# Performance work log

Hardware: AMD Instinct MI355X
Metric: run time of the kernel (lower is better)

## Reference

```python
import jax, jax.numpy as jnp
import numpy as np

B, S, D, H, FF = 2, 2048, 1024, 16, 4096
HD = D // H
EPS = 1e-5


def _ln(x, g, b):
    m = jnp.mean(x, axis=-1, keepdims=True)
    v = jnp.mean((x - m) ** 2, axis=-1, keepdims=True)
    return (x - m) * jax.lax.rsqrt(v + EPS) * g + b


def _rope(x, cos, sin):
    # non-standard RoPE: split full d_model at half, rotate (pre head-split)
    half = x.shape[-1] // 2
    x1, x2 = x[..., :half], x[..., half:]
    return jnp.concatenate([x1 * cos - x2 * sin, x1 * sin + x2 * cos], axis=-1)


def _heads(x, b, s):
    return x.reshape(b, s, H, HD).transpose(0, 2, 1, 3)  # [b,h,s,hd]


def _attn(q, k, v):
    scores = jnp.einsum('bhqd,bhkd->bhqk', q, k) / jnp.sqrt(jnp.float32(HD))
    w = jax.nn.softmax(scores, axis=-1)
    return jnp.einsum('bhqk,bhkd->bhqd', w, v)


def setup_inputs() -> dict:
    key = jax.random.key(0)
    ks = jax.random.split(key, 32)
    sc = 0.02
    d = {
        'x': jax.random.normal(ks[0], (B, S, D), jnp.float32),
        'cond_emb': jax.random.normal(ks[1], (B, D), jnp.float32),
    }
    # proper RoPE tables over half_dim = D//2
    pos = np.arange(S)[:, None]
    inv = 1.0 / (10000.0 ** (np.arange(D // 2) / (D // 2)))
    ang = pos * inv[None, :]
    d['cos_pos'] = jnp.asarray(np.cos(ang), jnp.float32)
    d['sin_pos'] = jnp.asarray(np.sin(ang), jnp.float32)
    names = ['Wq', 'Wk', 'Wv', 'Wo', 'Wqc', 'Wkc', 'Wvc', 'Woc']
    for i, n in enumerate(names):
        d[n] = jax.random.normal(ks[2 + i], (D, D), jnp.float32) * sc
        d['b' + n[1:]] = jnp.zeros((D,), jnp.float32)
    d['W1'] = jax.random.normal(ks[12], (D, FF), jnp.float32) * sc
    d['b1'] = jnp.zeros((FF,), jnp.float32)
    d['W2'] = jax.random.normal(ks[13], (FF, D), jnp.float32) * sc
    d['b2'] = jnp.zeros((D,), jnp.float32)
    for i in (1, 2, 3):
        d[f'g{i}'] = jnp.ones((D,), jnp.float32)
        d[f'be{i}'] = jnp.zeros((D,), jnp.float32)
    return d


def reference(x, cond_emb, cos_pos, sin_pos,
              Wq, bq, Wk, bk, Wv, bv, Wo, bo,
              Wqc, bqc, Wkc, bkc, Wvc, bvc, Woc, boc,
              W1, b1, W2, b2, g1, be1, g2, be2, g3, be3):
    b, s, _ = x.shape
    # self-attention with RoPE applied on full d_model before head split
    residual = x
    xn = _ln(x, g1, be1)
    q = _rope(xn @ Wq + bq, cos_pos, sin_pos)
    k = _rope(xn @ Wk + bk, cos_pos, sin_pos)
    v = xn @ Wv + bv
    o = _attn(_heads(q, b, s), _heads(k, b, s), _heads(v, b, s))
    o = o.transpose(0, 2, 1, 3).reshape(b, s, D) @ Wo + bo
    x = residual + o
    # cross-attention with single-token context
    residual = x
    xn = _ln(x, g2, be2)
    cond = cond_emb[:, None, :]  # [b,1,D]
    qc = _heads(xn @ Wqc + bqc, b, s)
    kc = _heads(cond @ Wkc + bkc, b, 1)
    vc = _heads(cond @ Wvc + bvc, b, 1)
    oc = _attn(qc, kc, vc)
    oc = oc.transpose(0, 2, 1, 3).reshape(b, s, D) @ Woc + boc
    x = residual + oc
    # FFN (exact GELU)
    residual = x
    xn = _ln(x, g3, be3)
    h = jax.nn.gelu(xn @ W1 + b1, approximate=False)
    return residual + (h @ W2 + b2)
```

## Files before the change

kernel.cpp:

```cpp
#include <hip/hip_runtime.h>
#include <cmath>

#define B_  2
#define S_  2048
#define D_  1024
#define H_  16
#define HD_ 64
#define FF_ 4096
#define M_  4096

typedef __attribute__((ext_vector_type(8))) __bf16 bf16x8;
typedef __attribute__((ext_vector_type(4))) __bf16 bf16x4;
typedef __attribute__((ext_vector_type(4))) float  f32x4;

__device__ __forceinline__ void gload_lds16(void* lds, const void* g) {
    __builtin_amdgcn_global_load_lds(
        (const __attribute__((address_space(1))) unsigned int*)g,
        (__attribute__((address_space(3))) unsigned int*)lds,
        16, 0, 0);
}

#define FENCE() asm volatile("" ::: "memory")

__global__ __launch_bounds__(256)
void tcast(const float* __restrict__ src, __bf16* __restrict__ dst, int K, int N)
{
    __shared__ float t[32][33];
    int tx = threadIdx.x & 31, ty = threadIdx.x >> 5;
    int k0 = blockIdx.y * 32, n0 = blockIdx.x * 32;
#pragma unroll
    for (int i = 0; i < 4; ++i)
        t[ty + i * 8][tx] = src[(size_t)(k0 + ty + i * 8) * N + n0 + tx];
    __syncthreads();
#pragma unroll
    for (int i = 0; i < 4; ++i)
        dst[(size_t)(n0 + ty + i * 8) * K + k0 + tx] = (__bf16)t[tx][ty + i * 8];
}

__global__ __launch_bounds__(256)
void tcast3(const float* __restrict__ wa, const float* __restrict__ wb,
            const float* __restrict__ wc, __bf16* __restrict__ dstb)
{
    __shared__ float t[32][33];
    const float* src = blockIdx.z == 0 ? wa : (blockIdx.z == 1 ? wb : wc);
    __bf16* dst = dstb + (size_t)blockIdx.z * 1024 * 1024;
    int tx = threadIdx.x & 31, ty = threadIdx.x >> 5;
    int k0 = blockIdx.y * 32, n0 = blockIdx.x * 32;
#pragma unroll
    for (int i = 0; i < 4; ++i)
        t[ty + i * 8][tx] = src[(size_t)(k0 + ty + i * 8) * 1024 + n0 + tx];
    __syncthreads();
#pragma unroll
    for (int i = 0; i < 4; ++i)
        dst[(size_t)(n0 + ty + i * 8) * 1024 + k0 + tx] = (__bf16)t[tx][ty + i * 8];
}

__global__ __launch_bounds__(256)
void catb(const float* __restrict__ a, const float* __restrict__ b,
          const float* __restrict__ c, float* __restrict__ o)
{
    int i = blockIdx.x * 256 + threadIdx.x;
    o[i] = i < 1024 ? a[i] : (i < 2048 ? b[i - 1024] : c[i - 2048]);
}

__global__ __launch_bounds__(256)
void colgemv(const float* __restrict__ inp, const float* __restrict__ W,
             const float* __restrict__ bias, float* __restrict__ out, int K, int N)
{
    __shared__ float part[4][16];
    const int b = blockIdx.y;
    const int t = threadIdx.x;
    const int w = t >> 6, lane = t & 63;
    const int colIdx = lane & 15;
    const int col = blockIdx.x * 16 + colIdx;
    const int ks = w * 4 + (lane >> 4);
    const int kpt = K >> 4;
    const float* ip = inp + (size_t)b * K + ks * kpt;
    const float* wp = W + (size_t)ks * kpt * N + col;
    float acc = 0.f;
#pragma unroll 8
    for (int i = 0; i < kpt; ++i)
        acc += ip[i] * wp[(size_t)i * N];
    acc += __shfl_xor(acc, 16);
    acc += __shfl_xor(acc, 32);
    if (lane < 16) part[w][colIdx] = acc;
    __syncthreads();
    if (t < 16) {
        float r = part[0][t] + part[1][t] + part[2][t] + part[3][t]
                + bias[blockIdx.x * 16 + t];
        out[(size_t)b * N + blockIdx.x * 16 + t] = r;
    }
}

__global__ __launch_bounds__(256)
void ln_cast(const float* __restrict__ x, const float* __restrict__ g,
             const float* __restrict__ be, __bf16* __restrict__ out)
{
    int row = blockIdx.x, tid = threadIdx.x;
    const float4* xp = (const float4*)(x + (size_t)row * D_);
    float4 v = xp[tid];
    float s  = v.x + v.y + v.z + v.w;
    float s2 = v.x * v.x + v.y * v.y + v.z * v.z + v.w * v.w;
#pragma unroll
    for (int off = 32; off > 0; off >>= 1) {
        s  += __shfl_down(s, off);
        s2 += __shfl_down(s2, off);
    }
    __shared__ float rs[4], rs2[4];
    int wid = tid >> 6, lane = tid & 63;
    if (lane == 0) { rs[wid] = s; rs2[wid] = s2; }
    __syncthreads();
    float tot  = rs[0] + rs[1] + rs[2] + rs[3];
    float tot2 = rs2[0] + rs2[1] + rs2[2] + rs2[3];
    float mean = tot * (1.0f / D_);
    float var  = tot2 * (1.0f / D_) - mean * mean;
    float rstd = rsqrtf(var + 1e-5f);
    float4 gv = ((const float4*)g)[tid];
    float4 bv = ((const float4*)be)[tid];
    bf16x4 ov;
    ov[0] = (__bf16)((v.x - mean) * rstd * gv.x + bv.x);
    ov[1] = (__bf16)((v.y - mean) * rstd * gv.y + bv.y);
    ov[2] = (__bf16)((v.z - mean) * rstd * gv.z + bv.z);
    ov[3] = (__bf16)((v.w - mean) * rstd * gv.w + bv.w);
    ((bf16x4*)(out + (size_t)row * D_))[tid] = ov;
}

__global__ __launch_bounds__(128)
void rope_qk(const __bf16* __restrict__ qkv, const float* __restrict__ cosp,
             const float* __restrict__ sinp, __bf16* __restrict__ Qh,
             __bf16* __restrict__ Kh)
{
    int row = blockIdx.x, tid = threadIdx.x;
    int b = row >> 11, s = row & 2047;
    float4 c  = ((const float4*)(cosp + (size_t)s * 512))[tid];
    float4 sn = ((const float4*)(sinp + (size_t)s * 512))[tid];
    int d0 = tid * 4;
    int h1 = d0 >> 6, dd = d0 & 63;
#pragma unroll
    for (int which = 0; which < 2; ++which) {
        const int off = which * 1024;
        const float scale = which ? 1.0f : 0.125f;
        __bf16* out = which ? Kh : Qh;
        bf16x4 a  = *(const bf16x4*)(qkv + (size_t)row * 3072 + off + tid * 4);
        bf16x4 bb = *(const bf16x4*)(qkv + (size_t)row * 3072 + off + 512 + tid * 4);
        float x1a = (float)a[0],  x1b = (float)a[1],  x1c = (float)a[2],  x1d = (float)a[3];
        float x2a = (float)bb[0], x2b = (float)bb[1], x2c = (float)bb[2], x2d = (float)bb[3];
        bf16x4 o1, o2;
        o1[0] = (__bf16)((x1a * c.x - x2a * sn.x) * scale);
        o1[1] = (__bf16)((x1b * c.y - x2b * sn.y) * scale);
        o1[2] = (__bf16)((x1c * c.z - x2c * sn.z) * scale);
        o1[3] = (__bf16)((x1d * c.w - x2d * sn.w) * scale);
        o2[0] = (__bf16)((x1a * sn.x + x2a * c.x) * scale);
        o2[1] = (__bf16)((x1b * sn.y + x2b * c.y) * scale);
        o2[2] = (__bf16)((x1c * sn.z + x2c * c.z) * scale);
        o2[3] = (__bf16)((x1d * sn.w + x2d * c.w) * scale);
        *(bf16x4*)(out + ((size_t)((b * H_ + h1) * S_ + s) * HD_) + dd) = o1;
        *(bf16x4*)(out + ((size_t)((b * H_ + h1 + 8) * S_ + s) * HD_) + dd) = o2;
    }
}

__global__ __launch_bounds__(256)
void vtrans2(const __bf16* __restrict__ qkv, __bf16* __restrict__ Vt)
{
    __shared__ __bf16 t[32][33];
    int tx = threadIdx.x & 31, ty = threadIdx.x >> 5;
    int bh = blockIdx.z;
    int b = bh >> 4, h = bh & 15;
    int s0 = blockIdx.y * 32, d0 = blockIdx.x * 32;
    __bf16* dst = Vt + (size_t)bh * HD_ * S_;
#pragma unroll
    for (int i = 0; i < 4; ++i)
        t[ty + i * 8][tx] = qkv[(size_t)(b * 2048 + s0 + ty + i * 8) * 3072
                                + 2048 + h * 64 + d0 + tx];
    __syncthreads();
#pragma unroll
    for (int i = 0; i < 4; ++i)
        dst[(size_t)(d0 + ty + i * 8) * S_ + s0 + tx] = t[tx][ty + i * 8];
}

template<int EPI>
__global__ __launch_bounds__(512)
void gemm8(const __bf16* __restrict__ A, const __bf16* __restrict__ Bt,
           const float* __restrict__ bias, __bf16* __restrict__ o0,
           __bf16* __restrict__ o1, int M, int N, int K, int klen)
{
    __shared__ __align__(16) char smem[131072];
    const int tid = threadIdx.x;
    const int wid = tid >> 6, lane = tid & 63;
    const int l15 = lane & 15, l16 = lane >> 4;
    const int wm = wid >> 2, wn = wid & 3;

    const int gx = gridDim.x;
    const int nwg = gx * gridDim.y;
    int wg = blockIdx.y * gx + blockIdx.x;
    wg = (wg & 7) * (nwg >> 3) + (wg >> 3);
    const int n0 = (wg % gx) * 256;
    const int m0 = (wg / gx) * 256;
    const int kz = blockIdx.z * klen;
    const size_t K2 = (size_t)K * 2;

    const int srow = tid >> 3;
    const int scol = ((tid & 7) * 16) ^ ((srow & 7) << 4);
    const char* gA = (const char*)A + (size_t)(m0 + srow) * K2 + (size_t)kz * 2 + scol;
    const char* gB = (const char*)Bt + (size_t)(n0 + srow) * K2 + (size_t)kz * 2 + scol;

    auto stageA = [&](int c) {
        char* d = (char*)smem + c * 32768 + wid * 1024;
        gload_lds16(d,         gA);
        gload_lds16(d + 8192,  gA + 64 * K2);
        gload_lds16(d + 16384, gA + 128 * K2);
        gload_lds16(d + 24576, gA + 192 * K2);
    };
    auto stageB = [&](int c) {
        char* d = (char*)smem + 65536 + c * 32768 + wid * 1024;
        gload_lds16(d,         gB);
        gload_lds16(d + 8192,  gB + 64 * K2);
        gload_lds16(d + 16384, gB + 128 * K2);
        gload_lds16(d + 24576, gB + 192 * K2);
    };

    const int sw = (l15 & 7) << 4;
    const int x0 = (l16 * 16) ^ sw;
    const int x1 = (64 + l16 * 16) ^ sw;
    const int aoff = (wm * 128 + l15) * 128;
    const int boff = 65536 + (wn * 64 + l15) * 128;

    f32x4 acc[8][4] = {};
    const int NT = klen >> 6;

    stageA(0); stageB(0); gA += 128; gB += 128;
    stageA(1); stageB(1); gA += 128; gB += 128;
    asm volatile("s_waitcnt vmcnt(8)" ::: "memory");
    __builtin_amdgcn_s_barrier();

    for (int t = 0; t < NT; ++t) {
        const int cur = t & 1;
        const char* sa = (const char*)smem + cur * 32768;
        const bool pf = (t + 2) < NT;

        bf16x8 af0[8], af1[8];
        bf16x8 b00, b01, b02, b03, b10, b11, b12, b13;

#pragma unroll
        for (int mi = 0; mi < 8; ++mi)
            af0[mi] = *(const bf16x8*)(sa + aoff + mi * 2048 + x0);
        b00 = *(const bf16x8*)(sa + boff + 0 * 2048 + x0);
        b01 = *(const bf16x8*)(sa + boff + 1 * 2048 + x0);
        FENCE();
        __builtin_amdgcn_s_barrier();
        __builtin_amdgcn_s_setprio(1);
#pragma unroll
        for (int mi = 0; mi < 8; ++mi) {
            acc[mi][0] = __builtin_amdgcn_mfma_f32_16x16x32_bf16(af0[mi], b00, acc[mi][0], 0, 0, 0);
            acc[mi][1] = __builtin_amdgcn_mfma_f32_16x16x32_bf16(af0[mi], b01, acc[mi][1], 0, 0, 0);
        }
        __builtin_amdgcn_s_setprio(0);

#pragma unroll
        for (int mi = 0; mi < 8; ++mi)
            af1[mi] = *(const bf16x8*)(sa + aoff + mi * 2048 + x1);
        b02 = *(const bf16x8*)(sa + boff + 2 * 2048 + x0);
        b03 = *(const bf16x8*)(sa + boff + 3 * 2048 + x0);
        FENCE();
        __builtin_amdgcn_s_barrier();
        __builtin_amdgcn_s_setprio(1);
#pragma unroll
        for (int mi = 0; mi < 8; ++mi) {
            acc[mi][2] = __builtin_amdgcn_mfma_f32_16x16x32_bf16(af0[mi], b02, acc[mi][2], 0, 0, 0);
            acc[mi][3] = __builtin_amdgcn_mfma_f32_16x16x32_bf16(af0[mi], b03, acc[mi][3], 0, 0, 0);
        }
        __builtin_amdgcn_s_setprio(0);

        b10 = *(const bf16x8*)(sa + boff + 0 * 2048 + x1);
        b11 = *(const bf16x8*)(sa + boff + 1 * 2048 + x1);
        FENCE();
        __builtin_amdgcn_s_barrier();
        if (pf) stageA(cur);
        __builtin_amdgcn_s_setprio(1);
#pragma unroll
        for (int mi = 0; mi < 8; ++mi) {
            acc[mi][0] = __builtin_amdgcn_mfma_f32_16x16x32_bf16(af1[mi], b10, acc[mi][0], 0, 0, 0);
            acc[mi][1] = __builtin_amdgcn_mfma_f32_16x16x32_bf16(af1[mi], b11, acc[mi][1], 0, 0, 0);
        }
        __builtin_amdgcn_s_setprio(0);

        b12 = *(const bf16x8*)(sa + boff + 2 * 2048 + x1);
        b13 = *(const bf16x8*)(sa + boff + 3 * 2048 + x1);
        FENCE();
        __builtin_amdgcn_s_barrier();
        if (pf) { stageB(cur); gA += 128; gB += 128; }
        __builtin_amdgcn_s_setprio(1);
#pragma unroll
        for (int mi = 0; mi < 8; ++mi) {
            acc[mi][2] = __builtin_amdgcn_mfma_f32_16x16x32_bf16(af1[mi], b12, acc[mi][2], 0, 0, 0);
            acc[mi][3] = __builtin_amdgcn_mfma_f32_16x16x32_bf16(af1[mi], b13, acc[mi][3], 0, 0, 0);
        }
        __builtin_amdgcn_s_setprio(0);
        if (pf) asm volatile("s_waitcnt vmcnt(8)" ::: "memory");
        else    asm volatile("s_waitcnt vmcnt(0)" ::: "memory");
        __builtin_amdgcn_s_barrier();
        FENCE();
    }

#pragma unroll
    for (int mi = 0; mi < 8; ++mi)
#pragma unroll
        for (int ni = 0; ni < 4; ++ni) {
            int gc = n0 + wn * 64 + ni * 16 + l15;
            float bb = (EPI == 2) ? 0.f : bias[gc];
#pragma unroll
            for (int r = 0; r < 4; ++r) {
                int gr = m0 + wm * 128 + mi * 16 + l16 * 4 + r;
                float v = acc[mi][ni][r] + bb;
                if constexpr (EPI == 0) {
                    o0[(size_t)gr * N + gc] = (__bf16)v;
                } else if constexpr (EPI == 1) {
                    o0[(size_t)gr * N + gc] =
                        (__bf16)(0.5f * v * (1.0f + erff(v * 0.70710678118f)));
                } else {
                    const size_t PSZ = (size_t)M_ * 1024;
                    __bf16* po = (blockIdx.z < 2) ? (o0 + blockIdx.z * PSZ)
                                                  : (o1 + (blockIdx.z - 2) * PSZ);
                    po[(size_t)gr * N + gc] = (__bf16)v;
                }
            }
        }
}

__global__ __launch_bounds__(256)
void ffn2_red(const __bf16* __restrict__ pA, const __bf16* __restrict__ pB,
              const float* __restrict__ x2, const float* __restrict__ b2,
              float* __restrict__ out)
{
    const size_t PSZ = (size_t)M_ * 1024;
    size_t i = ((size_t)blockIdx.x * 256 + threadIdx.x) * 8;
    bf16x8 a0 = *(const bf16x8*)(pA + i);
    bf16x8 a1 = *(const bf16x8*)(pA + PSZ + i);
    bf16x8 c0 = *(const bf16x8*)(pB + i);
    bf16x8 c1 = *(const bf16x8*)(pB + PSZ + i);
    float4 xa = *(const float4*)(x2 + i);
    float4 xb = *(const float4*)(x2 + i + 4);
    float xs[8] = {xa.x, xa.y, xa.z, xa.w, xb.x, xb.y, xb.z, xb.w};
#pragma unroll
    for (int j = 0; j < 8; ++j) {
        int col = (int)((i + j) & 1023);
        out[i + j] = xs[j] + b2[col]
                   + (float)a0[j] + (float)a1[j] + (float)c0[j] + (float)c1[j];
    }
}

__global__ __launch_bounds__(256)
void gemm_bt(const __bf16* __restrict__ A, const __bf16* __restrict__ Bt,
             const float* __restrict__ bias, const float* __restrict__ resid,
             const float* __restrict__ extra, float* __restrict__ outF,
             int M, int N, int K)
{
    __shared__ __align__(16) __bf16 As[128 * 64];
    __shared__ __align__(16) __bf16 Bs[128 * 64];
    const int tid = threadIdx.x;
    const int wid = tid >> 6, lane = tid & 63;
    const int m0 = blockIdx.y * 128, n0 = blockIdx.x * 128;
    const int wm = wid >> 1, wn = wid & 1;
    const int l15 = lane & 15, l16 = lane >> 4;

    f32x4 acc[4][4] = {};
    char* asb = (char*)As;
    char* bsb = (char*)Bs;
    const char* ag = (const char*)A;
    const char* bg = (const char*)Bt;
    const int srow = lane >> 3;
    const int scolsw = ((lane & 7) * 16) ^ (srow << 4);

    for (int k0 = 0; k0 < K; k0 += 64) {
        __syncthreads();
#pragma unroll
        for (int i = 0; i < 4; ++i) {
            int j = wid * 4 + i;
            int row = j * 8 + srow;
            gload_lds16(asb + j * 1024,
                        ag + (size_t)(m0 + row) * (K * 2) + k0 * 2 + scolsw);
        }
#pragma unroll
        for (int i = 0; i < 4; ++i) {
            int j = wid * 4 + i;
            int row = j * 8 + srow;
            gload_lds16(bsb + j * 1024,
                        bg + (size_t)(n0 + row) * (K * 2) + k0 * 2 + scolsw);
        }
        __syncthreads();

        bf16x8 af[4][2], bfr[4][2];
#pragma unroll
        for (int mi = 0; mi < 4; ++mi) {
            int row = wm * 64 + mi * 16 + l15;
            int swl = (row & 7) << 4;
#pragma unroll
            for (int kk = 0; kk < 2; ++kk)
                af[mi][kk] = *(const bf16x8*)(asb + row * 128 + ((l16 * 16 + kk * 64) ^ swl));
        }
#pragma unroll
        for (int ni = 0; ni < 4; ++ni) {
            int row = wn * 64 + ni * 16 + l15;
            int swl = (row & 7) << 4;
#pragma unroll
            for (int kk = 0; kk < 2; ++kk)
                bfr[ni][kk] = *(const bf16x8*)(bsb + row * 128 + ((l16 * 16 + kk * 64) ^ swl));
        }
#pragma unroll
        for (int mi = 0; mi < 4; ++mi)
#pragma unroll
            for (int ni = 0; ni < 4; ++ni) {
                acc[mi][ni] = __builtin_amdgcn_mfma_f32_16x16x32_bf16(af[mi][0], bfr[ni][0], acc[mi][ni], 0, 0, 0);
                acc[mi][ni] = __builtin_amdgcn_mfma_f32_16x16x32_bf16(af[mi][1], bfr[ni][1], acc[mi][ni], 0, 0, 0);
            }
    }

#pragma unroll
    for (int mi = 0; mi < 4; ++mi)
#pragma unroll
        for (int ni = 0; ni < 4; ++ni) {
            int gc = n0 + wn * 64 + ni * 16 + l15;
            float bb = bias[gc];
#pragma unroll
            for (int r = 0; r < 4; ++r) {
                int gr = m0 + wm * 64 + mi * 16 + l16 * 4 + r;
                float v = acc[mi][ni][r] + bb;
                size_t idx = (size_t)gr * N + gc;
                int b = gr >> 11;
                outF[idx] = resid[idx] + v + extra[(size_t)b * N + gc];
            }
        }
}

__global__ __launch_bounds__(256)
void attn_fwd(const __bf16* __restrict__ Qh, const __bf16* __restrict__ Kh,
              const __bf16* __restrict__ Vt, __bf16* __restrict__ O)
{
    __shared__ __align__(16) char smem[40960];
    const int tid = threadIdx.x, wid = tid >> 6, lane = tid & 63;
    const int l15 = lane & 15, l16 = lane >> 4;

    const int wg = blockIdx.x;
    const int rr = wg >> 3;
    const int qb = rr & 31;
    const int bh = (wg & 7) + 8 * (rr >> 5);

    const int q0 = qb * 64 + wid * 16;
    const size_t qkbase = (size_t)bh * S_ * HD_;

    bf16x8 qf[2];
    {
        const __bf16* qp = Qh + qkbase + (size_t)(q0 + l15) * HD_ + l16 * 8;
        qf[0] = *(const bf16x8*)qp;
        qf[1] = *(const bf16x8*)(qp + 32);
    }
    float m = -1e30f, sum = 0.f;
    f32x4 o[4] = {};
    const int srow = lane >> 3;
    const int scolsw = ((lane & 7) * 16) ^ (srow << 4);
    const char* kg = (const char*)(Kh + qkbase);
    const char* vg = (const char*)(Vt + (size_t)bh * HD_ * S_);

    auto stage = [&](int c, int t) {
        int s0 = t * 64;
#pragma unroll
        for (int cc = 0; cc < 2; ++cc) {
            int j = wid * 2 + cc;
            int row = j * 8 + srow;
            gload_lds16(smem + c * 8192 + j * 1024,
                        kg + (size_t)(s0 + row) * 128 + scolsw);
            gload_lds16(smem + 16384 + c * 8192 + j * 1024,
                        vg + (size_t)row * (S_ * 2) + s0 * 2 + scolsw);
        }
    };

    const int NT = S_ / 64;
    stage(0, 0);
    stage(1, 1);
    asm volatile("s_waitcnt vmcnt(4)" ::: "memory");
    __builtin_amdgcn_s_barrier();

    for (int kt = 0; kt < NT; ++kt) {
        const int cur = kt & 1;
        const char* Kl = smem + cur * 8192;
        const char* Vl = smem + 16384 + cur * 8192;
        char* Pl = smem + 32768;

        f32x4 st[4];
        __builtin_amdgcn_s_setprio(1);
#pragma unroll
        for (int t = 0; t < 4; ++t) {
            int row = t * 16 + l15;
            int swl = (row & 7) << 4;
            bf16x8 ak0 = *(const bf16x8*)(Kl + row * 128 + ((l16 * 16) ^ swl));
            bf16x8 ak1 = *(const bf16x8*)(Kl + row * 128 + ((l16 * 16 + 64) ^ swl));
            f32x4 z = {0.f, 0.f, 0.f, 0.f};
            z = __builtin_amdgcn_mfma_f32_16x16x32_bf16(ak0, qf[0], z, 0, 0, 0);
            st[t] = __builtin_amdgcn_mfma_f32_16x16x32_bf16(ak1, qf[1], z, 0, 0, 0);
        }
        __builtin_amdgcn_s_setprio(0);

        float rmax = -1e30f;
#pragma unroll
        for (int t = 0; t < 4; ++t)
#pragma unroll
            for (int r = 0; r < 4; ++r) rmax = fmaxf(rmax, st[t][r]);
        rmax = fmaxf(rmax, __shfl_xor(rmax, 16));
        rmax = fmaxf(rmax, __shfl_xor(rmax, 32));
        if (!__all(rmax <= m + 8.f)) {
            float mnew = fmaxf(m, rmax);
            float corr = __expf(m - mnew);
            sum *= corr;
            float c0 = __shfl(corr, l16 * 4 + 0);
            float c1 = __shfl(corr, l16 * 4 + 1);
            float c2 = __shfl(corr, l16 * 4 + 2);
            float c3 = __shfl(corr, l16 * 4 + 3);
#pragma unroll
            for (int dg = 0; dg < 4; ++dg) {
                o[dg][0] *= c0; o[dg][1] *= c1; o[dg][2] *= c2; o[dg][3] *= c3;
            }
            m = mnew;
        }
        float rsum = 0.f;
        float p[4][4];
#pragma unroll
        for (int t = 0; t < 4; ++t)
#pragma unroll
            for (int r = 0; r < 4; ++r) { p[t][r] = __expf(st[t][r] - m); rsum += p[t][r]; }
        rsum += __shfl_xor(rsum, 16);
        rsum += __shfl_xor(rsum, 32);
        sum += rsum;

        {
            char* pw = Pl + wid * 2048 + l15 * 128;
            int swl = (l15 & 7) << 4;
#pragma unroll
            for (int t = 0; t < 4; ++t) {
                bf16x4 pk;
                pk[0] = (__bf16)p[t][0]; pk[1] = (__bf16)p[t][1];
                pk[2] = (__bf16)p[t][2]; pk[3] = (__bf16)p[t][3];
                *(bf16x4*)(pw + ((t * 32 + l16 * 8) ^ swl)) = pk;
            }
        }
        {
            const char* pr = Pl + wid * 2048 + l15 * 128;
            int swp = (l15 & 7) << 4;
            bf16x8 ap0 = *(const bf16x8*)(pr + ((l16 * 16) ^ swp));
            bf16x8 ap1 = *(const bf16x8*)(pr + ((l16 * 16 + 64) ^ swp));
            __builtin_amdgcn_s_setprio(1);
#pragma unroll
            for (int dg = 0; dg < 4; ++dg) {
                int row = dg * 16 + l15;
                int swl = (row & 7) << 4;
                bf16x8 bv0 = *(const bf16x8*)(Vl + row * 128 + ((l16 * 16) ^ swl));
                bf16x8 bv1 = *(const bf16x8*)(Vl + row * 128 + ((l16 * 16 + 64) ^ swl));
                o[dg] = __builtin_amdgcn_mfma_f32_16x16x32_bf16(ap0, bv0, o[dg], 0, 0, 0);
                o[dg] = __builtin_amdgcn_mfma_f32_16x16x32_bf16(ap1, bv1, o[dg], 0, 0, 0);
            }
            __builtin_amdgcn_s_setprio(0);
        }

        FENCE();
        __builtin_amdgcn_s_barrier();
        if (kt + 2 < NT) {
            stage(cur, kt + 2);
            asm volatile("s_waitcnt vmcnt(4)" ::: "memory");
        } else {
            asm volatile("s_waitcnt vmcnt(0)" ::: "memory");
        }
        __builtin_amdgcn_s_barrier();
        FENCE();
    }

    int b = bh >> 4, hh = bh & 15;
#pragma unroll
    for (int r = 0; r < 4; ++r) {
        float inv = 1.0f / __shfl(sum, l16 * 4 + r);
        int qg = q0 + l16 * 4 + r;
        __bf16* op = O + ((size_t)(b * S_ + qg) * D_) + hh * HD_;
#pragma unroll
        for (int dg = 0; dg < 4; ++dg)
            op[dg * 16 + l15] = (__bf16)(o[dg][r] * inv);
    }
}

extern "C" void kernel_launch(void* const* d_in, const int* in_sizes, int n_in,
                              void* d_out, int out_size, void* d_ws, size_t ws_size,
                              hipStream_t stream)
{
    (void)in_sizes; (void)n_in; (void)out_size; (void)ws_size;
    const float* x    = (const float*)d_in[0];
    const float* cond = (const float*)d_in[1];
    const float* cosp = (const float*)d_in[2];
    const float* sinp = (const float*)d_in[3];
    const float* Wq = (const float*)d_in[4];  const float* bq = (const float*)d_in[5];
    const float* Wk = (const float*)d_in[6];  const float* bk = (const float*)d_in[7];
    const float* Wv = (const float*)d_in[8];  const float* bv = (const float*)d_in[9];
    const float* Wo = (const float*)d_in[10]; const float* bo = (const float*)d_in[11];
    const float* Wvc = (const float*)d_in[16]; const float* bvc = (const float*)d_in[17];
    const float* Woc = (const float*)d_in[18]; const float* boc = (const float*)d_in[19];
    const float* W1 = (const float*)d_in[20]; const float* b1 = (const float*)d_in[21];
    const float* W2 = (const float*)d_in[22]; const float* b2 = (const float*)d_in[23];
    const float* g1 = (const float*)d_in[24]; const float* be1 = (const float*)d_in[25];
    const float* g3 = (const float*)d_in[28]; const float* be3 = (const float*)d_in[29];

    char* ws = (char*)d_ws;
    const size_t MB = 1ull << 20;
    __bf16* WqkvT = (__bf16*)(ws + 0 * MB);
    __bf16* WoT   = (__bf16*)(ws + 6 * MB);
    __bf16* W1T   = (__bf16*)(ws + 8 * MB);
    __bf16* W2T   = (__bf16*)(ws + 16 * MB);
    __bf16* xn    = (__bf16*)(ws + 24 * MB);
    __bf16* qkvh  = (__bf16*)(ws + 32 * MB);
    __bf16* Qh    = (__bf16*)(ws + 56 * MB);
    __bf16* Kh    = (__bf16*)(ws + 64 * MB);
    __bf16* Vt    = (__bf16*)(ws + 72 * MB);
    __bf16* oflat = (__bf16*)(ws + 80 * MB);
    float*  bqkv  = (float*)(ws + 88 * MB);
    float*  vc    = (float*)(ws + 88 * MB + 16384);
    float*  ocp   = (float*)(ws + 88 * MB + 32768);
    float*  x2    = (float*)(ws + 32 * MB);
    __bf16* hbuf  = (__bf16*)(ws + 48 * MB);
    __bf16* pA    = (__bf16*)(ws + 0 * MB);
    __bf16* pB    = (__bf16*)(ws + 80 * MB);

    tcast3<<<dim3(32, 32, 3), 256, 0, stream>>>(Wq, Wk, Wv, WqkvT);
    tcast<<<dim3(32, 32),  256, 0, stream>>>(Wo, WoT, 1024, 1024);
    tcast<<<dim3(128, 32), 256, 0, stream>>>(W1, W1T, 1024, 4096);
    tcast<<<dim3(32, 128), 256, 0, stream>>>(W2, W2T, 4096, 1024);
    catb<<<12, 256, 0, stream>>>(bq, bk, bv, bqkv);
    colgemv<<<dim3(64, 2), 256, 0, stream>>>(cond, Wvc, bvc, vc, 1024, 1024);
    colgemv<<<dim3(64, 2), 256, 0, stream>>>(vc, Woc, boc, ocp, 1024, 1024);
    ln_cast<<<M_, 256, 0, stream>>>(x, g1, be1, xn);
    gemm8<0><<<dim3(12, 16, 1), 512, 0, stream>>>(xn, WqkvT, bqkv, qkvh, nullptr,
                                                  M_, 3072, 1024, 1024);
    rope_qk<<<M_, 128, 0, stream>>>(qkvh, cosp, sinp, Qh, Kh);
    vtrans2<<<dim3(2, 64, 32), 256, 0, stream>>>(qkvh, Vt);
    attn_fwd<<<1024, 256, 0, stream>>>(Qh, Kh, Vt, oflat);
    gemm_bt<<<dim3(8, 32), 256, 0, stream>>>(oflat, WoT, bo, x, ocp, x2,
                                             M_, 1024, 1024);
    ln_cast<<<M_, 256, 0, stream>>>(x2, g3, be3, xn);
    gemm8<1><<<dim3(16, 16, 1), 512, 0, stream>>>(xn, W1T, b1, hbuf, nullptr,
                                                  M_, 4096, 1024, 1024);
    gemm8<2><<<dim3(4, 16, 4), 512, 0, stream>>>(hbuf, W2T, nullptr, pA, pB,
                                                 M_, 1024, 4096, 1024);
    ffn2_red<<<2048, 256, 0, stream>>>(pA, pB, x2, b2, (float*)d_out);
}
```

Before: 274.3 us.

## Rewrite attention with 32x32 MFMA tiles, register-resident P, exp2 softmax

The flash-attention kernel moves from 16x16x32 to 32x32x16 MFMA tiles, so each wave handles 32 queries and each block 128, halving the grid. The P matrix no longer round-trips through shared memory: it is packed to bf16 in registers and rearranged with cross-half lane shuffles to form the B operand of the PV MFMA. Softmax switches to exp2 by folding log2(e) into the Q scale inside the RoPE kernel, and the lazy-rescale threshold is widened to match. This removes LDS traffic and per-row shuffles for the rescale factors, at the cost of more registers per wave and fewer blocks, which may lower occupancy.

```diff
diff --git a/kernel.cpp b/kernel.cpp
--- a/kernel.cpp
+++ b/kernel.cpp
@@ -12,6 +12,8 @@
 typedef __attribute__((ext_vector_type(8))) __bf16 bf16x8;
 typedef __attribute__((ext_vector_type(4))) __bf16 bf16x4;
 typedef __attribute__((ext_vector_type(4))) float  f32x4;
+typedef __attribute__((ext_vector_type(16))) float f32x16;
+typedef __attribute__((ext_vector_type(4))) unsigned u32x4;
 
 __device__ __forceinline__ void gload_lds16(void* lds, const void* g) {
     __builtin_amdgcn_global_load_lds(
@@ -21,6 +23,12 @@
 }
 
 #define FENCE() asm volatile("" ::: "memory")
+
+__device__ __forceinline__ unsigned pk_bf16(float lo, float hi) {
+    unsigned short lu = __builtin_bit_cast(unsigned short, (__bf16)lo);
+    unsigned short hu = __builtin_bit_cast(unsigned short, (__bf16)hi);
+    return (unsigned)lu | ((unsigned)hu << 16);
+}
 
 __global__ __launch_bounds__(256)
 void tcast(const float* __restrict__ src, __bf16* __restrict__ dst, int K, int N)
@@ -139,7 +147,7 @@
 #pragma unroll
     for (int which = 0; which < 2; ++which) {
         const int off = which * 1024;
-        const float scale = which ? 1.0f : 0.125f;
+        const float scale = which ? 1.0f : 0.18033688f;
         __bf16* out = which ? Kh : Qh;
         bf16x4 a  = *(const bf16x4*)(qkv + (size_t)row * 3072 + off + tid * 4);
         bf16x4 bb = *(const bf16x4*)(qkv + (size_t)row * 3072 + off + 512 + tid * 4);
@@ -436,28 +444,31 @@
 void attn_fwd(const __bf16* __restrict__ Qh, const __bf16* __restrict__ Kh,
               const __bf16* __restrict__ Vt, __bf16* __restrict__ O)
 {
-    __shared__ __align__(16) char smem[40960];
+    __shared__ __align__(16) char smem[32768];
     const int tid = threadIdx.x, wid = tid >> 6, lane = tid & 63;
-    const int l15 = lane & 15, l16 = lane >> 4;
+    const int l31 = lane & 31, hi = lane >> 5;
 
     const int wg = blockIdx.x;
     const int rr = wg >> 3;
-    const int qb = rr & 31;
-    const int bh = (wg & 7) + 8 * (rr >> 5);
-
-    const int q0 = qb * 64 + wid * 16;
+    const int qb = rr & 15;
+    const int bh = (wg & 7) + 8 * (rr >> 4);
+
+    const int qg = qb * 128 + wid * 32 + l31;
     const size_t qkbase = (size_t)bh * S_ * HD_;
 
-    bf16x8 qf[2];
+    bf16x8 qf[4];
     {
-        const __bf16* qp = Qh + qkbase + (size_t)(q0 + l15) * HD_ + l16 * 8;
-        qf[0] = *(const bf16x8*)qp;
-        qf[1] = *(const bf16x8*)(qp + 32);
-    }
+        const __bf16* qp = Qh + qkbase + (size_t)qg * HD_ + hi * 8;
+#pragma unroll
+        for (int kh = 0; kh < 4; ++kh)
+            qf[kh] = *(const bf16x8*)(qp + kh * 16);
+    }
+
     float m = -1e30f, sum = 0.f;
-    f32x4 o[4] = {};
+    f32x16 acc0 = {}, acc1 = {};
+
     const int srow = lane >> 3;
-    const int scolsw = ((lane & 7) * 16) ^ (srow << 4);
+    const int scolsw = ((lane & 7) * 16) ^ ((srow & 7) << 4);
     const char* kg = (const char*)(Kh + qkbase);
     const char* vg = (const char*)(Vt + (size_t)bh * HD_ * S_);
 
@@ -474,6 +485,8 @@
         }
     };
 
+    const int swz0 = (l31 & 7) << 4;
+
     const int NT = S_ / 64;
     stage(0, 0);
     stage(1, 1);
@@ -484,81 +497,72 @@
         const int cur = kt & 1;
         const char* Kl = smem + cur * 8192;
         const char* Vl = smem + 16384 + cur * 8192;
-        char* Pl = smem + 32768;
-
-        f32x4 st[4];
+
+        f32x16 st0 = {}, st1 = {};
         __builtin_amdgcn_s_setprio(1);
 #pragma unroll
-        for (int t = 0; t < 4; ++t) {
-            int row = t * 16 + l15;
-            int swl = (row & 7) << 4;
-            bf16x8 ak0 = *(const bf16x8*)(Kl + row * 128 + ((l16 * 16) ^ swl));
-            bf16x8 ak1 = *(const bf16x8*)(Kl + row * 128 + ((l16 * 16 + 64) ^ swl));
-            f32x4 z = {0.f, 0.f, 0.f, 0.f};
-            z = __builtin_amdgcn_mfma_f32_16x16x32_bf16(ak0, qf[0], z, 0, 0, 0);
-            st[t] = __builtin_amdgcn_mfma_f32_16x16x32_bf16(ak1, qf[1], z, 0, 0, 0);
+        for (int kh = 0; kh < 4; ++kh) {
+            int colb = kh * 32 + hi * 16;
+            bf16x8 k0 = *(const bf16x8*)(Kl + l31 * 128 + (colb ^ swz0));
+            bf16x8 k1 = *(const bf16x8*)(Kl + (32 + l31) * 128 + (colb ^ swz0));
+            st0 = __builtin_amdgcn_mfma_f32_32x32x16_bf16(k0, qf[kh], st0, 0, 0, 0);
+            st1 = __builtin_amdgcn_mfma_f32_32x32x16_bf16(k1, qf[kh], st1, 0, 0, 0);
         }
         __builtin_amdgcn_s_setprio(0);
 
-        float rmax = -1e30f;
-#pragma unroll
-        for (int t = 0; t < 4; ++t)
-#pragma unroll
-            for (int r = 0; r < 4; ++r) rmax = fmaxf(rmax, st[t][r]);
-        rmax = fmaxf(rmax, __shfl_xor(rmax, 16));
-        rmax = fmaxf(rmax, __shfl_xor(rmax, 32));
-        if (!__all(rmax <= m + 8.f)) {
-            float mnew = fmaxf(m, rmax);
-            float corr = __expf(m - mnew);
+        float rm = fmaxf(st0[0], st0[1]);
+#pragma unroll
+        for (int i = 2; i < 16; ++i) rm = fmaxf(rm, st0[i]);
+#pragma unroll
+        for (int i = 0; i < 16; ++i) rm = fmaxf(rm, st1[i]);
+        rm = fmaxf(rm, __shfl_xor(rm, 32));
+        if (!__all(rm <= m + 11.5f)) {
+            float mn = fmaxf(m, rm);
+            float corr = exp2f(m - mn);
             sum *= corr;
-            float c0 = __shfl(corr, l16 * 4 + 0);
-            float c1 = __shfl(corr, l16 * 4 + 1);
-            float c2 = __shfl(corr, l16 * 4 + 2);
-            float c3 = __shfl(corr, l16 * 4 + 3);
-#pragma unroll
-            for (int dg = 0; dg < 4; ++dg) {
-                o[dg][0] *= c0; o[dg][1] *= c1; o[dg][2] *= c2; o[dg][3] *= c3;
+            acc0 *= corr;
+            acc1 *= corr;
+            m = mn;
+        }
+        f32x16 p0, p1;
+        float rs = 0.f;
+#pragma unroll
+        for (int i = 0; i < 16; ++i) { p0[i] = exp2f(st0[i] - m); rs += p0[i]; }
+#pragma unroll
+        for (int i = 0; i < 16; ++i) { p1[i] = exp2f(st1[i] - m); rs += p1[i]; }
+        rs += __shfl_xor(rs, 32);
+        sum += rs;
+
+        unsigned pw[2][4][2];
+#pragma unroll
+        for (int g = 0; g < 4; ++g)
+#pragma unroll
+            for (int u = 0; u < 2; ++u) {
+                pw[0][g][u] = pk_bf16(p0[4 * g + 2 * u], p0[4 * g + 2 * u + 1]);
+                pw[1][g][u] = pk_bf16(p1[4 * g + 2 * u], p1[4 * g + 2 * u + 1]);
             }
-            m = mnew;
-        }
-        float rsum = 0.f;
-        float p[4][4];
-#pragma unroll
-        for (int t = 0; t < 4; ++t)
-#pragma unroll
-            for (int r = 0; r < 4; ++r) { p[t][r] = __expf(st[t][r] - m); rsum += p[t][r]; }
-        rsum += __shfl_xor(rsum, 16);
-        rsum += __shfl_xor(rsum, 32);
-        sum += rsum;
-
-        {
-            char* pw = Pl + wid * 2048 + l15 * 128;
-            int swl = (l15 & 7) << 4;
-#pragma unroll
-            for (int t = 0; t < 4; ++t) {
-                bf16x4 pk;
-                pk[0] = (__bf16)p[t][0]; pk[1] = (__bf16)p[t][1];
-                pk[2] = (__bf16)p[t][2]; pk[3] = (__bf16)p[t][3];
-                *(bf16x4*)(pw + ((t * 32 + l16 * 8) ^ swl)) = pk;
+
+        __builtin_amdgcn_s_setprio(1);
+#pragma unroll
+        for (int khp = 0; khp < 4; ++khp) {
+            const int s = khp >> 1, b0 = 2 * (khp & 1);
+            u32x4 tw;
+#pragma unroll
+            for (int u = 0; u < 2; ++u) {
+                unsigned a = pw[s][b0][u], b = pw[s][b0 + 1][u];
+                unsigned pa = (unsigned)__shfl_xor((int)a, 32);
+                unsigned pb = (unsigned)__shfl_xor((int)b, 32);
+                tw[u]     = hi ? pb : a;
+                tw[2 + u] = hi ? b  : pa;
             }
-        }
-        {
-            const char* pr = Pl + wid * 2048 + l15 * 128;
-            int swp = (l15 & 7) << 4;
-            bf16x8 ap0 = *(const bf16x8*)(pr + ((l16 * 16) ^ swp));
-            bf16x8 ap1 = *(const bf16x8*)(pr + ((l16 * 16 + 64) ^ swp));
-            __builtin_amdgcn_s_setprio(1);
-#pragma unroll
-            for (int dg = 0; dg < 4; ++dg) {
-                int row = dg * 16 + l15;
-                int swl = (row & 7) << 4;
-                bf16x8 bv0 = *(const bf16x8*)(Vl + row * 128 + ((l16 * 16) ^ swl));
-                bf16x8 bv1 = *(const bf16x8*)(Vl + row * 128 + ((l16 * 16 + 64) ^ swl));
-                o[dg] = __builtin_amdgcn_mfma_f32_16x16x32_bf16(ap0, bv0, o[dg], 0, 0, 0);
-                o[dg] = __builtin_amdgcn_mfma_f32_16x16x32_bf16(ap1, bv1, o[dg], 0, 0, 0);
-            }
-            __builtin_amdgcn_s_setprio(0);
-        }
+            bf16x8 pfrag = __builtin_bit_cast(bf16x8, tw);
+            int colb = khp * 32 + hi * 16;
+            bf16x8 v0 = *(const bf16x8*)(Vl + l31 * 128 + (colb ^ swz0));
+            bf16x8 v1 = *(const bf16x8*)(Vl + (32 + l31) * 128 + (colb ^ swz0));
+            acc0 = __builtin_amdgcn_mfma_f32_32x32x16_bf16(v0, pfrag, acc0, 0, 0, 0);
+            acc1 = __builtin_amdgcn_mfma_f32_32x32x16_bf16(v1, pfrag, acc1, 0, 0, 0);
+        }
+        __builtin_amdgcn_s_setprio(0);
 
         FENCE();
         __builtin_amdgcn_s_barrier();
@@ -572,15 +576,20 @@
         FENCE();
     }
 
+    float inv = 1.0f / sum;
     int b = bh >> 4, hh = bh & 15;
-#pragma unroll
-    for (int r = 0; r < 4; ++r) {
-        float inv = 1.0f / __shfl(sum, l16 * 4 + r);
-        int qg = q0 + l16 * 4 + r;
-        __bf16* op = O + ((size_t)(b * S_ + qg) * D_) + hh * HD_;
-#pragma unroll
-        for (int dg = 0; dg < 4; ++dg)
-            op[dg * 16 + l15] = (__bf16)(o[dg][r] * inv);
+    __bf16* op = O + ((size_t)(b * S_ + qg) * D_) + hh * HD_;
+#pragma unroll
+    for (int ds = 0; ds < 2; ++ds) {
+        f32x16 a = ds ? acc1 : acc0;
+#pragma unroll
+        for (int g = 0; g < 4; ++g) {
+            bf16x4 ov;
+#pragma unroll
+            for (int e = 0; e < 4; ++e)
+                ov[e] = (__bf16)(a[4 * g + e] * inv);
+            *(bf16x4*)(op + ds * 32 + g * 8 + hi * 4) = ov;
+        }
     }
 }
 
@@ -636,7 +645,7 @@
                                                   M_, 3072, 1024, 1024);
     rope_qk<<<M_, 128, 0, stream>>>(qkvh, cosp, sinp, Qh, Kh);
     vtrans2<<<dim3(2, 64, 32), 256, 0, stream>>>(qkvh, Vt);
-    attn_fwd<<<1024, 256, 0, stream>>>(Qh, Kh, Vt, oflat);
+    attn_fwd<<<512, 256, 0, stream>>>(Qh, Kh, Vt, oflat);
     gemm_bt<<<dim3(8, 32), 256, 0, stream>>>(oflat, WoT, bo, x, ocp, x2,
                                              M_, 1024, 1024);
     ln_cast<<<M_, 256, 0, stream>>>(x2, g3, be3, xn);
```

Result: slower. 287.4 us (+4.8%).

## Split attention over KV halves with 512-thread blocks and log-sum-exp merge

Applied to the files above, without the earlier changes.

Attention now splits the key sequence into two halves, each handled by a separate block of 8 waves covering 128 queries, and writes partial outputs plus log2-sum-exp values. A new merge kernel combines the two halves. Softmax switches to exp2 by folding log2(e) into the Q scale, and the max and sum reductions become tree-shaped. The goal is more K/V reuse per block and cheaper exponentials. The cost is an extra kernel launch and an extra round trip of the partial outputs through memory.

```diff
diff --git a/kernel.cpp b/kernel.cpp
--- a/kernel.cpp
+++ b/kernel.cpp
@@ -139,7 +139,7 @@
 #pragma unroll
     for (int which = 0; which < 2; ++which) {
         const int off = which * 1024;
-        const float scale = which ? 1.0f : 0.125f;
+        const float scale = which ? 1.0f : 0.18033688f;
         __bf16* out = which ? Kh : Qh;
         bf16x4 a  = *(const bf16x4*)(qkv + (size_t)row * 3072 + off + tid * 4);
         bf16x4 bb = *(const bf16x4*)(qkv + (size_t)row * 3072 + off + 512 + tid * 4);
@@ -432,20 +432,23 @@
         }
 }
 
-__global__ __launch_bounds__(256)
+__global__ __launch_bounds__(512)
 void attn_fwd(const __bf16* __restrict__ Qh, const __bf16* __restrict__ Kh,
-              const __bf16* __restrict__ Vt, __bf16* __restrict__ O)
-{
-    __shared__ __align__(16) char smem[40960];
+              const __bf16* __restrict__ Vt, __bf16* __restrict__ Op,
+              float* __restrict__ Lp)
+{
+    __shared__ __align__(16) char smem[49152];
     const int tid = threadIdx.x, wid = tid >> 6, lane = tid & 63;
     const int l15 = lane & 15, l16 = lane >> 4;
 
     const int wg = blockIdx.x;
     const int rr = wg >> 3;
-    const int qb = rr & 31;
+    const int qb = rr & 15;
+    const int split = (rr >> 4) & 1;
     const int bh = (wg & 7) + 8 * (rr >> 5);
-
-    const int q0 = qb * 64 + wid * 16;
+    const int kt0 = split * 16;
+
+    const int q0 = qb * 128 + wid * 16;
     const size_t qkbase = (size_t)bh * S_ * HD_;
 
     bf16x8 qf[2];
@@ -457,34 +460,30 @@
     float m = -1e30f, sum = 0.f;
     f32x4 o[4] = {};
     const int srow = lane >> 3;
-    const int scolsw = ((lane & 7) * 16) ^ (srow << 4);
+    const int scolsw = ((lane & 7) * 16) ^ ((srow & 7) << 4);
     const char* kg = (const char*)(Kh + qkbase);
     const char* vg = (const char*)(Vt + (size_t)bh * HD_ * S_);
 
     auto stage = [&](int c, int t) {
         int s0 = t * 64;
-#pragma unroll
-        for (int cc = 0; cc < 2; ++cc) {
-            int j = wid * 2 + cc;
-            int row = j * 8 + srow;
-            gload_lds16(smem + c * 8192 + j * 1024,
-                        kg + (size_t)(s0 + row) * 128 + scolsw);
-            gload_lds16(smem + 16384 + c * 8192 + j * 1024,
-                        vg + (size_t)row * (S_ * 2) + s0 * 2 + scolsw);
-        }
+        int row = wid * 8 + srow;
+        gload_lds16(smem + c * 8192 + wid * 1024,
+                    kg + (size_t)(s0 + row) * 128 + scolsw);
+        gload_lds16(smem + 16384 + c * 8192 + wid * 1024,
+                    vg + (size_t)row * (S_ * 2) + s0 * 2 + scolsw);
     };
 
-    const int NT = S_ / 64;
-    stage(0, 0);
-    stage(1, 1);
-    asm volatile("s_waitcnt vmcnt(4)" ::: "memory");
+    const int NT = 16;
+    stage(0, kt0);
+    stage(1, kt0 + 1);
+    asm volatile("s_waitcnt vmcnt(2)" ::: "memory");
     __builtin_amdgcn_s_barrier();
 
-    for (int kt = 0; kt < NT; ++kt) {
-        const int cur = kt & 1;
+    for (int ki = 0; ki < NT; ++ki) {
+        const int cur = ki & 1;
         const char* Kl = smem + cur * 8192;
         const char* Vl = smem + 16384 + cur * 8192;
-        char* Pl = smem + 32768;
+        char* Pl = smem + 32768 + wid * 2048;
 
         f32x4 st[4];
         __builtin_amdgcn_s_setprio(1);
@@ -500,16 +499,20 @@
         }
         __builtin_amdgcn_s_setprio(0);
 
-        float rmax = -1e30f;
-#pragma unroll
-        for (int t = 0; t < 4; ++t)
-#pragma unroll
-            for (int r = 0; r < 4; ++r) rmax = fmaxf(rmax, st[t][r]);
+        float t8[8];
+#pragma unroll
+        for (int i = 0; i < 4; ++i) {
+            t8[i]     = fmaxf(st[0][i], st[1][i]);
+            t8[4 + i] = fmaxf(st[2][i], st[3][i]);
+        }
+#pragma unroll
+        for (int i = 0; i < 4; ++i) t8[i] = fmaxf(t8[i], t8[i + 4]);
+        float rmax = fmaxf(fmaxf(t8[0], t8[1]), fmaxf(t8[2], t8[3]));
         rmax = fmaxf(rmax, __shfl_xor(rmax, 16));
         rmax = fmaxf(rmax, __shfl_xor(rmax, 32));
-        if (!__all(rmax <= m + 8.f)) {
+        if (!__all(rmax <= m + 11.5f)) {
             float mnew = fmaxf(m, rmax);
-            float corr = __expf(m - mnew);
+            float corr = exp2f(m - mnew);
             sum *= corr;
             float c0 = __shfl(corr, l16 * 4 + 0);
             float c1 = __shfl(corr, l16 * 4 + 1);
@@ -521,18 +524,26 @@
             }
             m = mnew;
         }
-        float rsum = 0.f;
         float p[4][4];
 #pragma unroll
         for (int t = 0; t < 4; ++t)
 #pragma unroll
-            for (int r = 0; r < 4; ++r) { p[t][r] = __expf(st[t][r] - m); rsum += p[t][r]; }
+            for (int r = 0; r < 4; ++r) p[t][r] = exp2f(st[t][r] - m);
+        float s8[8];
+#pragma unroll
+        for (int i = 0; i < 4; ++i) {
+            s8[i]     = p[0][i] + p[1][i];
+            s8[4 + i] = p[2][i] + p[3][i];
+        }
+#pragma unroll
+        for (int i = 0; i < 4; ++i) s8[i] += s8[i + 4];
+        float rsum = (s8[0] + s8[1]) + (s8[2] + s8[3]);
         rsum += __shfl_xor(rsum, 16);
         rsum += __shfl_xor(rsum, 32);
         sum += rsum;
 
         {
-            char* pw = Pl + wid * 2048 + l15 * 128;
+            char* pw = Pl + l15 * 128;
             int swl = (l15 & 7) << 4;
 #pragma unroll
             for (int t = 0; t < 4; ++t) {
@@ -543,7 +554,7 @@
             }
         }
         {
-            const char* pr = Pl + wid * 2048 + l15 * 128;
+            const char* pr = Pl + l15 * 128;
             int swp = (l15 & 7) << 4;
             bf16x8 ap0 = *(const bf16x8*)(pr + ((l16 * 16) ^ swp));
             bf16x8 ap1 = *(const bf16x8*)(pr + ((l16 * 16 + 64) ^ swp));
@@ -562,9 +573,9 @@
 
         FENCE();
         __builtin_amdgcn_s_barrier();
-        if (kt + 2 < NT) {
-            stage(cur, kt + 2);
-            asm volatile("s_waitcnt vmcnt(4)" ::: "memory");
+        if (ki + 2 < NT) {
+            stage(cur, kt0 + ki + 2);
+            asm volatile("s_waitcnt vmcnt(2)" ::: "memory");
         } else {
             asm volatile("s_waitcnt vmcnt(0)" ::: "memory");
         }
@@ -572,16 +583,44 @@
         FENCE();
     }
 
-    int b = bh >> 4, hh = bh & 15;
+    __bf16* ob = Op + ((size_t)split * 65536 + (size_t)bh * 2048) * 64;
 #pragma unroll
     for (int r = 0; r < 4; ++r) {
         float inv = 1.0f / __shfl(sum, l16 * 4 + r);
         int qg = q0 + l16 * 4 + r;
-        __bf16* op = O + ((size_t)(b * S_ + qg) * D_) + hh * HD_;
 #pragma unroll
         for (int dg = 0; dg < 4; ++dg)
-            op[dg * 16 + l15] = (__bf16)(o[dg][r] * inv);
-    }
+            ob[(size_t)qg * 64 + dg * 16 + l15] = (__bf16)(o[dg][r] * inv);
+    }
+    if (lane < 16)
+        Lp[(size_t)split * 65536 + (size_t)bh * 2048 + q0 + lane]
+            = m + log2f(sum);
+}
+
+__global__ __launch_bounds__(256)
+void attn_merge(const __bf16* __restrict__ Op, const float* __restrict__ Lp,
+                __bf16* __restrict__ O)
+{
+    int idx = blockIdx.x * 256 + threadIdx.x;
+    int bh = idx >> 14;
+    int rem = idx & 16383;
+    int s = rem >> 3;
+    int d0 = (rem & 7) * 8;
+    size_t qi = (size_t)bh * 2048 + s;
+    float L1 = Lp[qi], L2 = Lp[65536 + qi];
+    float Lm = fmaxf(L1, L2);
+    float w1 = exp2f(L1 - Lm), w2 = exp2f(L2 - Lm);
+    float inv = 1.0f / (w1 + w2);
+    w1 *= inv; w2 *= inv;
+    bf16x8 o1 = *(const bf16x8*)(Op + qi * 64 + d0);
+    bf16x8 o2 = *(const bf16x8*)(Op + (size_t)65536 * 64 + qi * 64 + d0);
+    int b = bh >> 4, h = bh & 15;
+    __bf16* op = O + ((size_t)(b * S_ + s) * D_) + h * 64 + d0;
+    bf16x8 ov;
+#pragma unroll
+    for (int j = 0; j < 8; ++j)
+        ov[j] = (__bf16)(w1 * (float)o1[j] + w2 * (float)o2[j]);
+    *(bf16x8*)op = ov;
 }
 
 extern "C" void kernel_launch(void* const* d_in, const int* in_sizes, int n_in,
@@ -619,6 +658,8 @@
     float*  bqkv  = (float*)(ws + 88 * MB);
     float*  vc    = (float*)(ws + 88 * MB + 16384);
     float*  ocp   = (float*)(ws + 88 * MB + 32768);
+    __bf16* Opart = (__bf16*)(ws + 32 * MB);
+    float*  Lpart = (float*)(ws + 48 * MB);
     float*  x2    = (float*)(ws + 32 * MB);
     __bf16* hbuf  = (__bf16*)(ws + 48 * MB);
     __bf16* pA    = (__bf16*)(ws + 0 * MB);
@@ -636,7 +677,8 @@
                                                   M_, 3072, 1024, 1024);
     rope_qk<<<M_, 128, 0, stream>>>(qkvh, cosp, sinp, Qh, Kh);
     vtrans2<<<dim3(2, 64, 32), 256, 0, stream>>>(qkvh, Vt);
-    attn_fwd<<<1024, 256, 0, stream>>>(Qh, Kh, Vt, oflat);
+    attn_fwd<<<1024, 512, 0, stream>>>(Qh, Kh, Vt, Opart, Lpart);
+    attn_merge<<<2048, 256, 0, stream>>>(Opart, Lpart, oflat);
     gemm_bt<<<dim3(8, 32), 256, 0, stream>>>(oflat, WoT, bo, x, ocp, x2,
                                              M_, 1024, 1024);
     ln_cast<<<M_, 256, 0, stream>>>(x2, g3, be3, xn);
```

Measured after the change: 280.0 us. +2.1%, slower.
